# Performance work log

Measured on AMD Instinct MI355X. Metric: run time of the kernel, lower is better.

The kernel has to match this reference:

```python
import jax, jax.numpy as jnp
import numpy as np

D_MODEL = 1024
NUM_HEADS = 16
ALPHA = 1.0


def setup_inputs() -> dict:
    key = jax.random.key(0)
    ks = jax.random.split(key, 6)
    bs, L, d = 2, 2048, D_MODEL
    s = 1.0 / np.sqrt(d)
    mu = jax.random.normal(ks[0], (bs, L, d), dtype=jnp.float32)
    sigma = jax.random.uniform(ks[1], (bs, L, d), dtype=jnp.float32)
    W_qkv_mu = (jax.random.normal(ks[2], (d, 3 * d), dtype=jnp.float32) * s)
    b_qkv_mu = jnp.zeros((3 * d,), dtype=jnp.float32)
    W_qkv_sigma = (jax.random.normal(ks[3], (d, 3 * d), dtype=jnp.float32) * s)
    b_qkv_sigma = jnp.zeros((3 * d,), dtype=jnp.float32)
    W_out = (jax.random.normal(ks[4], (d, d), dtype=jnp.float32) * s)
    b_out = jnp.zeros((d,), dtype=jnp.float32)
    return {"mu": mu, "sigma": sigma,
            "W_qkv_mu": W_qkv_mu, "b_qkv_mu": b_qkv_mu,
            "W_qkv_sigma": W_qkv_sigma, "b_qkv_sigma": b_qkv_sigma,
            "W_out": W_out, "b_out": b_out}


def reference(mu, sigma, W_qkv_mu, b_qkv_mu, W_qkv_sigma, b_qkv_sigma, W_out, b_out):
    bs, L, d = mu.shape
    H = NUM_HEADS
    dk = d // H

    def heads(x):  # [b, L, d] -> [b, H, L, dk]
        return x.reshape(bs, L, H, dk).transpose(0, 2, 1, 3)

    Qm, Km, Vm = (heads(t) for t in jnp.split(mu @ W_qkv_mu + b_qkv_mu, 3, axis=-1))
    Qs, Ks, Vs = (heads(t) for t in jnp.split(sigma @ W_qkv_sigma + b_qkv_sigma, 3, axis=-1))

    # Wasserstein^2 = sum((Qm-Km)^2) + sum((Qs-Ks)^2), expanded so the
    # pairwise [b,H,L,L,dk] broadcast tensor is never materialized.
    sq_q = jnp.sum(Qm * Qm, -1) + jnp.sum(Qs * Qs, -1)  # [b,H,L]
    sq_k = jnp.sum(Km * Km, -1) + jnp.sum(Ks * Ks, -1)  # [b,H,L]
    cross = (jnp.einsum('bhid,bhjd->bhij', Qm, Km)
             + jnp.einsum('bhid,bhjd->bhij', Qs, Ks))   # [b,H,L,L]
    W2 = sq_q[..., :, None] + sq_k[..., None, :] - 2.0 * cross
    W = jnp.sqrt(jnp.maximum(W2, 0.0))

    similarity = jnp.exp(-ALPHA * W)
    attn = jax.nn.softmax(similarity, axis=-1)  # softmax OVER the similarities (as in torch code)

    def merge(x):  # [b,H,L,dk] -> [b,L,d]
        return x.transpose(0, 2, 1, 3).reshape(bs, L, d)

    out_mu = merge(jnp.einsum('bhij,bhjd->bhid', attn, Vm)) @ W_out + b_out
    out_sigma = merge(jnp.einsum('bhij,bhjd->bhid', attn, Vs)) @ W_out + b_out
    return out_mu, out_sigma
```

## Files before the change

### kernel.cpp

```cpp
#include <hip/hip_runtime.h>
#include <hip/hip_bf16.h>

#define LSEQ   2048
#define DK     64
#define NH     16
#define BS     2
#define DMODEL 1024
#define BH     (BS*NH)
#define MTOT   (BS*LSEQ)

typedef __attribute__((ext_vector_type(8))) short bf16x8;
typedef __attribute__((ext_vector_type(4))) float f32x4;
typedef __attribute__((ext_vector_type(16))) float f32x16;

#define MFMA16(a,b,c) __builtin_amdgcn_mfma_f32_16x16x32_bf16((a),(b),(c),0,0,0)
#define MFMA32(a,b,c) __builtin_amdgcn_mfma_f32_32x32x16_bf16((a),(b),(c),0,0,0)
#define GLD_LDS(g,l) __builtin_amdgcn_global_load_lds((const __attribute__((address_space(1))) void*)(g), (__attribute__((address_space(3))) void*)(l), 16, 0, 0)

#define L2E   1.4426950408889634f
#define L2E2  2.0813689810056077f

__device__ __forceinline__ short f2bs(float f) {
  union { __hip_bfloat16 h; short s; } u; u.h = __float2bfloat16(f); return u.s;
}
__device__ __forceinline__ float b2f(unsigned short s) {
  union { unsigned u; float f; } v; v.u = ((unsigned)s) << 16; return v.f;
}
__device__ __forceinline__ unsigned short f2bs_c(float f) {
  union { float f; unsigned u; } v; v.f = f;
  return (unsigned short)((v.u + 0x8000u) >> 16);
}
__device__ __forceinline__ unsigned pk2c(float lo, float hi) {
  union { float f; unsigned u; } a, b; a.f = lo; b.f = hi;
  return ((a.u + 0x8000u) >> 16) | ((b.u + 0x8000u) & 0xffff0000u);
}
__device__ __forceinline__ unsigned pk2(float lo, float hi) {
  return (unsigned)(unsigned short)f2bs(lo) | (((unsigned)(unsigned short)f2bs(hi)) << 16);
}
__device__ __forceinline__ float fexp2(float x) {
  float r; asm("v_exp_f32 %0, %1" : "=v"(r) : "v"(x)); return r;
}
__device__ __forceinline__ float fexp2n(float x) {
  float r; asm("v_exp_f32 %0, -%1" : "=v"(r) : "v"(x)); return r;
}

__global__ __launch_bounds__(256) void cvt2_k(const float* __restrict__ a,
                                              const float* __restrict__ b,
                                              short* __restrict__ oa,
                                              short* __restrict__ ob, int n8) {
  int total = n8 * 2;
  for (int i = blockIdx.x * blockDim.x + threadIdx.x; i < total; i += gridDim.x * blockDim.x) {
    int sel = i >= n8;
    int j = sel ? i - n8 : i;
    const float4* p = (const float4*)(sel ? b : a) + (size_t)j * 2;
    float4 x = p[0], y = p[1];
    uint4 o;
    o.x = pk2(x.x, x.y); o.y = pk2(x.z, x.w);
    o.z = pk2(y.x, y.y); o.w = pk2(y.z, y.w);
    ((uint4*)(sel ? ob : oa))[j] = o;
  }
}

__global__ __launch_bounds__(256) void cvt_tr_all_k(
    const float* __restrict__ Wqm, const float* __restrict__ Wqs, const float* __restrict__ Wo,
    short* __restrict__ Wqm_t, short* __restrict__ Wqs_t, short* __restrict__ Wo_t) {
  __shared__ float tile[32][33];
  int id = blockIdx.x;
  const float* W; short* Wt; int Ncols, bx;
  if (id < 3072)      { W = Wqm; Wt = Wqm_t; Ncols = 3072; bx = id % 96; id /= 96; }
  else if (id < 6144) { id -= 3072; W = Wqs; Wt = Wqs_t; Ncols = 3072; bx = id % 96; id /= 96; }
  else                { id -= 6144; W = Wo;  Wt = Wo_t;  Ncols = 1024; bx = id % 32; id /= 32; }
  int n0 = bx * 32, k0 = id * 32;
  int t = threadIdx.x;
#pragma unroll
  for (int i = 0; i < 4; ++i) {
    int idx = t + i * 256; int r = idx >> 5, c = idx & 31;
    tile[r][c] = W[(size_t)(k0 + r) * Ncols + n0 + c];
  }
  __syncthreads();
#pragma unroll
  for (int i = 0; i < 4; ++i) {
    int idx = t + i * 256; int r = idx >> 5, c = idx & 31;
    Wt[(size_t)(n0 + r) * 1024 + k0 + c] = f2bs(tile[c][r]);
  }
}

__global__ __launch_bounds__(256) void qkv_gemm_k(
    const short* __restrict__ Amu, const short* __restrict__ Asg,
    const short* __restrict__ Wqm_t, const short* __restrict__ Wqs_t,
    const float* __restrict__ bqm, const float* __restrict__ bqs,
    short* __restrict__ Qm, short* __restrict__ Km, short* __restrict__ VmT,
    short* __restrict__ Qs, short* __restrict__ Ks, short* __restrict__ VsT) {
  __shared__ short As[128 * 64];
  __shared__ short Bs[128 * 64];
  int ny = blockIdx.y;
  int sg = ny >= 24;
  int n0 = (sg ? ny - 24 : ny) * 128;
  const short* A  = sg ? Asg : Amu;
  const short* Bt = sg ? Wqs_t : Wqm_t;
  const float* bias = sg ? bqs : bqm;
  short* Qb  = sg ? Qs : Qm;
  short* Kb  = sg ? Ks : Km;
  short* VTb = sg ? VsT : VmT;

  int tid = threadIdx.x, w = tid >> 6, ln = tid & 63, lg = ln >> 4, lr = ln & 15;
  int m0 = blockIdx.x * 128;
  int wr = w >> 1, wc = w & 1;
  f32x4 acc[4][4] = {};

  for (int k0 = 0; k0 < 1024; k0 += 64) {
    __syncthreads();
#pragma unroll
    for (int i = 0; i < 4; ++i) {
      int cb = w * 64 + i * 256;
      int c = cb + ln;
      GLD_LDS(A  + (size_t)(m0 + (c >> 3)) * 1024 + k0 + (c & 7) * 8, &As[cb * 8]);
      GLD_LDS(Bt + (size_t)(n0 + (c >> 3)) * 1024 + k0 + (c & 7) * 8, &Bs[cb * 8]);
    }
    __syncthreads();
#pragma unroll
    for (int kh = 0; kh < 2; ++kh) {
      bf16x8 af[4], bfr[4];
#pragma unroll
      for (int mi = 0; mi < 4; ++mi)
        af[mi] = *(const bf16x8*)&As[(wr * 64 + mi * 16 + lr) * 64 + kh * 32 + lg * 8];
#pragma unroll
      for (int ni = 0; ni < 4; ++ni)
        bfr[ni] = *(const bf16x8*)&Bs[(wc * 64 + ni * 16 + lr) * 64 + kh * 32 + lg * 8];
#pragma unroll
      for (int mi = 0; mi < 4; ++mi)
#pragma unroll
        for (int ni = 0; ni < 4; ++ni)
          acc[mi][ni] = MFMA16(af[mi], bfr[ni], acc[mi][ni]);
    }
  }

#pragma unroll
  for (int ni = 0; ni < 4; ++ni) {
    int n = n0 + wc * 64 + ni * 16 + lr;
    float bv = bias[n];
    int part = n >> 10, cc = n & 1023, hh = cc >> 6, dd = cc & 63;
#pragma unroll
    for (int mi = 0; mi < 4; ++mi) {
      int mbase = m0 + wr * 64 + mi * 16 + 4 * lg;
      float vv[4];
#pragma unroll
      for (int r = 0; r < 4; ++r) vv[r] = acc[mi][ni][r] + bv;
      if (part == 2) {
        int b = mbase >> 11, tok = mbase & 2047, bh = b * NH + hh;
        uint2 pk; pk.x = pk2c(vv[0], vv[1]); pk.y = pk2c(vv[2], vv[3]);
        *(uint2*)&VTb[((size_t)bh * DK + dd) * LSEQ + tok] = pk;
      } else {
        short* dst = (part == 0) ? Qb : Kb;
#pragma unroll
        for (int r = 0; r < 4; ++r) {
          int m = mbase + r;
          int b = m >> 11, tok = m & 2047, bh = b * NH + hh;
          dst[((size_t)bh * LSEQ + tok) * DK + dd] = (short)f2bs_c(vv[r]);
        }
      }
    }
  }
}

__global__ __launch_bounds__(256) void gemm128_k(
    const short* __restrict__ A, const short* __restrict__ Bt,
    const float* __restrict__ bias, float* __restrict__ outF) {
  __shared__ short As[128 * 64];
  __shared__ short Bs[128 * 64];
  int tid = threadIdx.x, w = tid >> 6, ln = tid & 63, lg = ln >> 4, lr = ln & 15;
  int m0 = blockIdx.x * 128, n0 = blockIdx.y * 128;
  int wr = w >> 1, wc = w & 1;
  f32x4 acc[4][4] = {};

  for (int k0 = 0; k0 < 1024; k0 += 64) {
    __syncthreads();
#pragma unroll
    for (int i = 0; i < 4; ++i) {
      int cb = w * 64 + i * 256;
      int c = cb + ln;
      GLD_LDS(A  + (size_t)(m0 + (c >> 3)) * 1024 + k0 + (c & 7) * 8, &As[cb * 8]);
      GLD_LDS(Bt + (size_t)(n0 + (c >> 3)) * 1024 + k0 + (c & 7) * 8, &Bs[cb * 8]);
    }
    __syncthreads();
#pragma unroll
    for (int kh = 0; kh < 2; ++kh) {
      bf16x8 af[4], bfr[4];
#pragma unroll
      for (int mi = 0; mi < 4; ++mi)
        af[mi] = *(const bf16x8*)&As[(wr * 64 + mi * 16 + lr) * 64 + kh * 32 + lg * 8];
#pragma unroll
      for (int ni = 0; ni < 4; ++ni)
        bfr[ni] = *(const bf16x8*)&Bs[(wc * 64 + ni * 16 + lr) * 64 + kh * 32 + lg * 8];
#pragma unroll
      for (int mi = 0; mi < 4; ++mi)
#pragma unroll
        for (int ni = 0; ni < 4; ++ni)
          acc[mi][ni] = MFMA16(af[mi], bfr[ni], acc[mi][ni]);
    }
  }

#pragma unroll
  for (int ni = 0; ni < 4; ++ni) {
    int n = n0 + wc * 64 + ni * 16 + lr;
    float bv = bias[n];
#pragma unroll
    for (int mi = 0; mi < 4; ++mi) {
      int mbase = m0 + wr * 64 + mi * 16 + 4 * lg;
#pragma unroll
      for (int r = 0; r < 4; ++r)
        outF[(size_t)(mbase + r) * 1024 + n] = acc[mi][ni][r] + bv;
    }
  }
}

__global__ __launch_bounds__(256) void norms_k(
    const short* __restrict__ Qm, const short* __restrict__ Qs,
    const short* __restrict__ Km, const short* __restrict__ Ks,
    float* __restrict__ sqq, float* __restrict__ sqk) {
  int id = blockIdx.x * 256 + threadIdx.x;
  int row = id & 65535;
  const short* p1 = (id < 65536) ? Qm : Km;
  const short* p2 = (id < 65536) ? Qs : Ks;
  float* outp = (id < 65536) ? sqq : sqk;
  const uint4* a = (const uint4*)(p1 + (size_t)row * DK);
  const uint4* b = (const uint4*)(p2 + (size_t)row * DK);
  float s = 0.f;
#pragma unroll
  for (int i = 0; i < 8; ++i) {
    uint4 x = a[i], y = b[i];
    unsigned vx[4] = {x.x, x.y, x.z, x.w};
    unsigned vy[4] = {y.x, y.y, y.z, y.w};
#pragma unroll
    for (int j = 0; j < 4; ++j) {
      float l1 = b2f((unsigned short)(vx[j] & 0xffff)), h1 = b2f((unsigned short)(vx[j] >> 16));
      float l2 = b2f((unsigned short)(vy[j] & 0xffff)), h2 = b2f((unsigned short)(vy[j] >> 16));
      s += l1 * l1 + h1 * h1 + l2 * l2 + h2 * h2;
    }
  }
  outp[row] = s * L2E2;
}

__global__ __launch_bounds__(512, 2) void attn_k(
    const short* __restrict__ Qm, const short* __restrict__ Km, const short* __restrict__ VmT,
    const short* __restrict__ Qs, const short* __restrict__ Ks, const short* __restrict__ VsT,
    const float* __restrict__ sqq, const float* __restrict__ sqk,
    short* __restrict__ Om, short* __restrict__ Os) {
  int id = blockIdx.y * 8 + blockIdx.x;
  int pid = id >> 3;
  int bh = (id & 7) * 4 + (pid >> 3);
  int q0 = (pid & 7) * 256;
  int tid = threadIdx.x, w = tid >> 6, ln = tid & 63;
  int l31 = ln & 31, h = ln >> 5;

  __shared__ __align__(16) char pool[65536];
  short* poolS = (short*)pool;

  const size_t bhQ = (size_t)bh * LSEQ * DK;

  int q = q0 + w * 32 + l31;
  bf16x8 qmf[4], qsf[4];
#pragma unroll
  for (int d = 0; d < 4; ++d) {
    qmf[d] = *(const bf16x8*)(Qm + bhQ + (size_t)q * DK + d * 16 + h * 8);
    qsf[d] = *(const bf16x8*)(Qs + bhQ + (size_t)q * DK + d * 16 + h * 8);
  }
  float sqQ = sqq[(size_t)bh * LSEQ + q];
  const float* sqkp = sqk + (size_t)bh * LSEQ;

  const short* sb0;
  {
    int t2 = tid & 255;
    int rr = t2 >> 3;
    int cs = ((t2 & 7) ^ (rr & 7) ^ ((rr >> 3) & 3)) * 8;
    sb0 = ((tid < 256) ? Km : Ks) + bhQ + (size_t)rr * DK + cs;
  }
  const short* sb1;
  {
    int rv = tid >> 2, sv = tid & 3;
    int cs = (sv ^ ((rv >> 1) & 3)) * 8;
    sb1 = ((rv < 64) ? (VmT + ((size_t)bh * DK + rv) * LSEQ)
                     : (VsT + ((size_t)bh * DK + (rv - 64)) * LSEQ)) + cs;
  }

  f32x16 acc[4] = {};
  float prs = 0.f;

  const int krow = l31;
  const int kswz = ((krow & 7) ^ ((krow >> 3) & 3)) << 4;

#pragma unroll
  for (int p = 0; p < 3; ++p) {
    GLD_LDS(sb0 + (size_t)p * 2048, poolS + p * 8192 + w * 512);
    GLD_LDS(sb1 + (size_t)p * 32,   poolS + p * 8192 + 4096 + w * 512);
  }

  const int NT = LSEQ / 32;
  for (int t = 0; t < NT; ++t) {
    asm volatile("s_waitcnt vmcnt(4)" ::: "memory");
    asm volatile("s_barrier" ::: "memory");
    {
      int tn = (t + 3 < NT) ? (t + 3) : (NT - 1);
      int bn = (t + 3) & 3;
      GLD_LDS(sb0 + (size_t)tn * 2048, poolS + bn * 8192 + w * 512);
      GLD_LDS(sb1 + (size_t)tn * 32,   poolS + bn * 8192 + 4096 + w * 512);
    }
    const char* base = (const char*)(poolS + (t & 3) * 8192);

    f32x16 sm = {}, ss = {};
    __builtin_amdgcn_s_setprio(1);
#pragma unroll
    for (int d = 0; d < 4; ++d) {
      bf16x8 am = *(const bf16x8*)(base + krow * 128 + ((d * 32 + h * 16) ^ kswz));
      bf16x8 as = *(const bf16x8*)(base + 4096 + krow * 128 + ((d * 32 + h * 16) ^ kswz));
      sm = MFMA32(am, qmf[d], sm);
      ss = MFMA32(as, qsf[d], ss);
    }
    __builtin_amdgcn_s_setprio(0);

    float pv[16];
    int k0b = t * 32;
#pragma unroll
    for (int rq = 0; rq < 4; ++rq) {
      f32x4 rsk = *(const f32x4*)&sqkp[k0b + 8 * rq + 4 * h];
#pragma unroll
      for (int r = 0; r < 4; ++r) {
        int i = rq * 4 + r;
        float w2 = fmaf(-2.f * L2E2, sm[i] + ss[i], sqQ + rsk[r]);
        float wdp = __builtin_amdgcn_sqrtf(fmaxf(w2, 0.f));
        float sim = fexp2n(wdp);
        float p = fexp2(sim * L2E);
        prs += p;
        pv[i] = p;
      }
    }
    unsigned u0 = pk2c(pv[0], pv[1]),   u1 = pk2c(pv[2], pv[3]);
    unsigned u2 = pk2c(pv[4], pv[5]),   u3 = pk2c(pv[6], pv[7]);
    unsigned u4 = pk2c(pv[8], pv[9]),   u5 = pk2c(pv[10], pv[11]);
    unsigned u6 = pk2c(pv[12], pv[13]), u7 = pk2c(pv[14], pv[15]);
    asm volatile("v_permlane32_swap_b32 %0, %1" : "+v"(u0), "+v"(u2));
    asm volatile("v_permlane32_swap_b32 %0, %1" : "+v"(u1), "+v"(u3));
    asm volatile("v_permlane32_swap_b32 %0, %1" : "+v"(u4), "+v"(u6));
    asm volatile("v_permlane32_swap_b32 %0, %1" : "+v"(u5), "+v"(u7));
    union { uint4 u; bf16x8 v; } f0, f1;
    f0.u.x = u0; f0.u.y = u1; f0.u.z = u2; f0.u.w = u3;
    f1.u.x = u4; f1.u.y = u5; f1.u.z = u6; f1.u.w = u7;

    __builtin_amdgcn_s_setprio(1);
#pragma unroll
    for (int vblk = 0; vblk < 4; ++vblk) {
      int vrow = vblk * 32 + l31;
      int vswz = ((vrow >> 1) & 3) << 4;
      const char* vbase = base + 8192 + vrow * 64;
      bf16x8 v0 = *(const bf16x8*)(vbase + ((h * 16) ^ vswz));
      bf16x8 v1 = *(const bf16x8*)(vbase + ((32 + h * 16) ^ vswz));
      acc[vblk] = MFMA32(v0, f0.v, acc[vblk]);
      acc[vblk] = MFMA32(v1, f1.v, acc[vblk]);
    }
    __builtin_amdgcn_s_setprio(0);
  }

  asm volatile("s_waitcnt vmcnt(0)" ::: "memory");

  prs += __shfl_xor(prs, 32);
  float inv = 1.f / prs;

  int b = bh >> 4, hh = bh & 15;
  size_t orow = ((size_t)(b * LSEQ + q)) * DMODEL + hh * DK;
#pragma unroll
  for (int vblk = 0; vblk < 4; ++vblk) {
    short* obuf = (vblk < 2) ? Om : Os;
    int vbase = (vblk & 1) * 32 + 4 * h;
#pragma unroll
    for (int rq = 0; rq < 4; ++rq) {
      float o0 = acc[vblk][rq * 4 + 0] * inv;
      float o1 = acc[vblk][rq * 4 + 1] * inv;
      float o2 = acc[vblk][rq * 4 + 2] * inv;
      float o3 = acc[vblk][rq * 4 + 3] * inv;
      uint2 pk; pk.x = pk2c(o0, o1); pk.y = pk2c(o2, o3);
      *(uint2*)(obuf + orow + vbase + 8 * rq) = pk;
    }
  }
}

extern "C" void kernel_launch(void* const* d_in, const int* in_sizes, int n_in,
                              void* d_out, int out_size, void* d_ws, size_t ws_size,
                              hipStream_t stream) {
  const float* mu    = (const float*)d_in[0];
  const float* sigma = (const float*)d_in[1];
  const float* Wqm   = (const float*)d_in[2];
  const float* bqm   = (const float*)d_in[3];
  const float* Wqs   = (const float*)d_in[4];
  const float* bqs   = (const float*)d_in[5];
  const float* Wo    = (const float*)d_in[6];
  const float* bo    = (const float*)d_in[7];
  float* out = (float*)d_out;
  char* ws = (char*)d_ws;
  const size_t MB = 1u << 20;

  short* Amu   = (short*)(ws + 0);
  short* Asg   = (short*)(ws + 8 * MB);
  short* Wqm_t = (short*)(ws + 16 * MB);
  short* Wqs_t = (short*)(ws + 22 * MB);
  short* Wo_t  = (short*)(ws + 28 * MB);
  short* Qm    = (short*)(ws + 30 * MB);
  short* Km    = (short*)(ws + 38 * MB);
  short* VmT   = (short*)(ws + 46 * MB);
  short* Qs    = (short*)(ws + 54 * MB);
  short* Ks    = (short*)(ws + 62 * MB);
  short* VsT   = (short*)(ws + 70 * MB);
  float* sqq   = (float*)(ws + 78 * MB);
  float* sqk   = (float*)(ws + 78 * MB + 256 * 1024);
  short* Om = Amu;
  short* Os = Asg;

  cvt2_k<<<2048, 256, 0, stream>>>(mu, sigma, Amu, Asg, MTOT * DMODEL / 8);
  cvt_tr_all_k<<<7168, 256, 0, stream>>>(Wqm, Wqs, Wo, Wqm_t, Wqs_t, Wo_t);

  qkv_gemm_k<<<dim3(32, 48), 256, 0, stream>>>(Amu, Asg, Wqm_t, Wqs_t, bqm, bqs,
                                               Qm, Km, VmT, Qs, Ks, VsT);

  norms_k<<<512, 256, 0, stream>>>(Qm, Qs, Km, Ks, sqq, sqk);

  attn_k<<<dim3(8, 32), 512, 0, stream>>>(Qm, Km, VmT, Qs, Ks, VsT, sqq, sqk, Om, Os);

  gemm128_k<<<dim3(64, 8), 256, 0, stream>>>(Om, Wo_t, bo, out);
}
```

Before: 259.4 us.

## Software-pipeline QK and PV across tiles in Wasserstein attention loop

Restructures the attention main loop so the QK MFMAs for tile t are issued while the softmax and PV MFMAs consume tile t-1, with a prologue and epilogue. It merges the mu and sigma score accumulators into one MFMA chain, prefetches squared key norms into registers one tile ahead, and changes the V tile LDS layout and swizzle to 128-byte rows. It also replaces the manual bf16 rounding with the hardware v_cvt_pk_bf16_f32 instruction. The pipeline prefetch distance drops from 3 to 2 tiles, and the extra live accumulators raise register pressure.

```diff
diff --git a/kernel.cpp b/kernel.cpp
--- a/kernel.cpp
+++ b/kernel.cpp
@@ -42,6 +42,9 @@
 }
 __device__ __forceinline__ float fexp2n(float x) {
   float r; asm("v_exp_f32 %0, -%1" : "=v"(r) : "v"(x)); return r;
+}
+__device__ __forceinline__ unsigned cvtpk(float lo, float hi) {
+  unsigned r; asm("v_cvt_pk_bf16_f32 %0, %1, %2" : "=v"(r) : "v"(lo), "v"(hi)); return r;
 }
 
 __global__ __launch_bounds__(256) void cvt2_k(const float* __restrict__ a,
@@ -277,10 +280,10 @@
   }
   const short* sb1;
   {
-    int rv = tid >> 2, sv = tid & 3;
-    int cs = (sv ^ ((rv >> 1) & 3)) * 8;
-    sb1 = ((rv < 64) ? (VmT + ((size_t)bh * DK + rv) * LSEQ)
-                     : (VsT + ((size_t)bh * DK + (rv - 64)) * LSEQ)) + cs;
+    int row = tid >> 3;
+    int c = (tid & 7) ^ (row & 7);
+    sb1 = ((c < 4) ? (VmT + ((size_t)bh * DK + row) * LSEQ + c * 8)
+                   : (VsT + ((size_t)bh * DK + row) * LSEQ + (c - 4) * 8));
   }
 
   f32x16 acc[4] = {};
@@ -288,45 +291,57 @@
 
   const int krow = l31;
   const int kswz = ((krow & 7) ^ ((krow >> 3) & 3)) << 4;
-
-#pragma unroll
-  for (int p = 0; p < 3; ++p) {
-    GLD_LDS(sb0 + (size_t)p * 2048, poolS + p * 8192 + w * 512);
-    GLD_LDS(sb1 + (size_t)p * 32,   poolS + p * 8192 + 4096 + w * 512);
-  }
-
   const int NT = LSEQ / 32;
-  for (int t = 0; t < NT; ++t) {
-    asm volatile("s_waitcnt vmcnt(4)" ::: "memory");
+
+#define ISSUE_TILE(tt, bb) do {                                          \
+    GLD_LDS(sb0 + (size_t)(tt) * 2048, poolS + (bb) * 8192 + w * 512);   \
+    GLD_LDS(sb1 + (size_t)(tt) * 32,   poolS + (bb) * 8192 + 4096 + w * 512); \
+  } while (0)
+
+#define QK_TILE(bb, sdst) do {                                           \
+    const char* kb_ = (const char*)(poolS + (bb) * 8192);                \
+    __builtin_amdgcn_s_setprio(1);                                       \
+    _Pragma("unroll")                                                    \
+    for (int d = 0; d < 4; ++d) {                                        \
+      bf16x8 am = *(const bf16x8*)(kb_ + krow * 128 + ((d * 32 + h * 16) ^ kswz)); \
+      sdst = MFMA32(am, qmf[d], sdst);                                   \
+      bf16x8 as = *(const bf16x8*)(kb_ + 4096 + krow * 128 + ((d * 32 + h * 16) ^ kswz)); \
+      sdst = MFMA32(as, qsf[d], sdst);                                   \
+    }                                                                    \
+    __builtin_amdgcn_s_setprio(0);                                       \
+  } while (0)
+
+  ISSUE_TILE(0, 0);
+  ISSUE_TILE(1, 1);
+  asm volatile("s_waitcnt vmcnt(2)" ::: "memory");
+  asm volatile("s_barrier" ::: "memory");
+  ISSUE_TILE(2, 2);
+
+  f32x16 s_prev = {};
+  QK_TILE(0, s_prev);
+  f32x4 rskreg[4];
+#pragma unroll
+  for (int rq = 0; rq < 4; ++rq)
+    rskreg[rq] = *(const f32x4*)&sqkp[8 * rq + 4 * h];
+
+  for (int t = 1; t < NT; ++t) {
+    asm volatile("s_waitcnt vmcnt(6)" ::: "memory");
     asm volatile("s_barrier" ::: "memory");
     {
-      int tn = (t + 3 < NT) ? (t + 3) : (NT - 1);
-      int bn = (t + 3) & 3;
-      GLD_LDS(sb0 + (size_t)tn * 2048, poolS + bn * 8192 + w * 512);
-      GLD_LDS(sb1 + (size_t)tn * 32,   poolS + bn * 8192 + 4096 + w * 512);
-    }
-    const char* base = (const char*)(poolS + (t & 3) * 8192);
-
-    f32x16 sm = {}, ss = {};
-    __builtin_amdgcn_s_setprio(1);
-#pragma unroll
-    for (int d = 0; d < 4; ++d) {
-      bf16x8 am = *(const bf16x8*)(base + krow * 128 + ((d * 32 + h * 16) ^ kswz));
-      bf16x8 as = *(const bf16x8*)(base + 4096 + krow * 128 + ((d * 32 + h * 16) ^ kswz));
-      sm = MFMA32(am, qmf[d], sm);
-      ss = MFMA32(as, qsf[d], ss);
-    }
-    __builtin_amdgcn_s_setprio(0);
+      int tn = (t + 2 < NT) ? (t + 2) : (NT - 1);
+      ISSUE_TILE(tn, (t + 2) & 3);
+    }
+
+    f32x16 s_cur = {};
+    QK_TILE(t & 3, s_cur);
 
     float pv[16];
-    int k0b = t * 32;
 #pragma unroll
     for (int rq = 0; rq < 4; ++rq) {
-      f32x4 rsk = *(const f32x4*)&sqkp[k0b + 8 * rq + 4 * h];
 #pragma unroll
       for (int r = 0; r < 4; ++r) {
         int i = rq * 4 + r;
-        float w2 = fmaf(-2.f * L2E2, sm[i] + ss[i], sqQ + rsk[r]);
+        float w2 = fmaf(-2.f * L2E2, s_prev[i], sqQ + rskreg[rq][r]);
         float wdp = __builtin_amdgcn_sqrtf(fmaxf(w2, 0.f));
         float sim = fexp2n(wdp);
         float p = fexp2(sim * L2E);
@@ -334,10 +349,10 @@
         pv[i] = p;
       }
     }
-    unsigned u0 = pk2c(pv[0], pv[1]),   u1 = pk2c(pv[2], pv[3]);
-    unsigned u2 = pk2c(pv[4], pv[5]),   u3 = pk2c(pv[6], pv[7]);
-    unsigned u4 = pk2c(pv[8], pv[9]),   u5 = pk2c(pv[10], pv[11]);
-    unsigned u6 = pk2c(pv[12], pv[13]), u7 = pk2c(pv[14], pv[15]);
+    unsigned u0 = cvtpk(pv[0], pv[1]),   u1 = cvtpk(pv[2], pv[3]);
+    unsigned u2 = cvtpk(pv[4], pv[5]),   u3 = cvtpk(pv[6], pv[7]);
+    unsigned u4 = cvtpk(pv[8], pv[9]),   u5 = cvtpk(pv[10], pv[11]);
+    unsigned u6 = cvtpk(pv[12], pv[13]), u7 = cvtpk(pv[14], pv[15]);
     asm volatile("v_permlane32_swap_b32 %0, %1" : "+v"(u0), "+v"(u2));
     asm volatile("v_permlane32_swap_b32 %0, %1" : "+v"(u1), "+v"(u3));
     asm volatile("v_permlane32_swap_b32 %0, %1" : "+v"(u4), "+v"(u6));
@@ -346,21 +361,72 @@
     f0.u.x = u0; f0.u.y = u1; f0.u.z = u2; f0.u.w = u3;
     f1.u.x = u4; f1.u.y = u5; f1.u.z = u6; f1.u.w = u7;
 
-    __builtin_amdgcn_s_setprio(1);
+#pragma unroll
+    for (int rq = 0; rq < 4; ++rq)
+      rskreg[rq] = *(const f32x4*)&sqkp[t * 32 + 8 * rq + 4 * h];
+
+    {
+      const char* vb = (const char*)(poolS + ((t - 1) & 3) * 8192) + 8192;
+      __builtin_amdgcn_s_setprio(1);
+#pragma unroll
+      for (int vblk = 0; vblk < 4; ++vblk) {
+        int row = (vblk & 1) * 32 + l31;
+        int cb = (vblk >> 1) * 4;
+        int sw = row & 7;
+        const char* rb = vb + row * 128;
+        bf16x8 v0 = *(const bf16x8*)(rb + (((cb + h) ^ sw) << 4));
+        bf16x8 v1 = *(const bf16x8*)(rb + (((cb + 2 + h) ^ sw) << 4));
+        acc[vblk] = MFMA32(v0, f0.v, acc[vblk]);
+        acc[vblk] = MFMA32(v1, f1.v, acc[vblk]);
+      }
+      __builtin_amdgcn_s_setprio(0);
+    }
+
+    s_prev = s_cur;
+  }
+
+  asm volatile("s_waitcnt vmcnt(0)" ::: "memory");
+
+  {
+    float pv[16];
+#pragma unroll
+    for (int rq = 0; rq < 4; ++rq) {
+#pragma unroll
+      for (int r = 0; r < 4; ++r) {
+        int i = rq * 4 + r;
+        float w2 = fmaf(-2.f * L2E2, s_prev[i], sqQ + rskreg[rq][r]);
+        float wdp = __builtin_amdgcn_sqrtf(fmaxf(w2, 0.f));
+        float sim = fexp2n(wdp);
+        float p = fexp2(sim * L2E);
+        prs += p;
+        pv[i] = p;
+      }
+    }
+    unsigned u0 = cvtpk(pv[0], pv[1]),   u1 = cvtpk(pv[2], pv[3]);
+    unsigned u2 = cvtpk(pv[4], pv[5]),   u3 = cvtpk(pv[6], pv[7]);
+    unsigned u4 = cvtpk(pv[8], pv[9]),   u5 = cvtpk(pv[10], pv[11]);
+    unsigned u6 = cvtpk(pv[12], pv[13]), u7 = cvtpk(pv[14], pv[15]);
+    asm volatile("v_permlane32_swap_b32 %0, %1" : "+v"(u0), "+v"(u2));
+    asm volatile("v_permlane32_swap_b32 %0, %1" : "+v"(u1), "+v"(u3));
+    asm volatile("v_permlane32_swap_b32 %0, %1" : "+v"(u4), "+v"(u6));
+    asm volatile("v_permlane32_swap_b32 %0, %1" : "+v"(u5), "+v"(u7));
+    union { uint4 u; bf16x8 v; } f0, f1;
+    f0.u.x = u0; f0.u.y = u1; f0.u.z = u2; f0.u.w = u3;
+    f1.u.x = u4; f1.u.y = u5; f1.u.z = u6; f1.u.w = u7;
+
+    const char* vb = (const char*)(poolS + ((NT - 1) & 3) * 8192) + 8192;
 #pragma unroll
     for (int vblk = 0; vblk < 4; ++vblk) {
-      int vrow = vblk * 32 + l31;
-      int vswz = ((vrow >> 1) & 3) << 4;
-      const char* vbase = base + 8192 + vrow * 64;
-      bf16x8 v0 = *(const bf16x8*)(vbase + ((h * 16) ^ vswz));
-      bf16x8 v1 = *(const bf16x8*)(vbase + ((32 + h * 16) ^ vswz));
+      int row = (vblk & 1) * 32 + l31;
+      int cb = (vblk >> 1) * 4;
+      int sw = row & 7;
+      const char* rb = vb + row * 128;
+      bf16x8 v0 = *(const bf16x8*)(rb + (((cb + h) ^ sw) << 4));
+      bf16x8 v1 = *(const bf16x8*)(rb + (((cb + 2 + h) ^ sw) << 4));
       acc[vblk] = MFMA32(v0, f0.v, acc[vblk]);
       acc[vblk] = MFMA32(v1, f1.v, acc[vblk]);
     }
-    __builtin_amdgcn_s_setprio(0);
-  }
-
-  asm volatile("s_waitcnt vmcnt(0)" ::: "memory");
+  }
 
   prs += __shfl_xor(prs, 32);
   float inv = 1.f / prs;
@@ -381,6 +447,8 @@
       *(uint2*)(obuf + orow + vbase + 8 * rq) = pk;
     }
   }
+#undef ISSUE_TILE
+#undef QK_TILE
 }
 
 extern "C" void kernel_launch(void* const* d_in, const int* in_sizes, int n_in,
```

Result: faster. 234.1 us (-9.8%).
